# Optimization experiments

Measured on AMD Instinct MI355X. Metric: run time of the kernel, lower is better.

## Reference

```python
import jax, jax.numpy as jnp
import numpy as np

RES = 128
SH_DIM = 9            # (deg+1)^2, deg=2
CH = SH_DIM * 3 + 1   # 28: 3*9 SH rgb coeffs + 1 sigma
AABB_MIN = -1.0
AABB_MAX = 1.0
STEP = (AABB_MAX - AABB_MIN) / (RES - 1)   # voxel_len = mean(aabb_size/(res-1))
UNIFORM = 0.5
N_SAMPLES = int(RES * 3 / UNIFORM)         # plenoxels count: 768
EPS = 1e-10


def sh_encode_deg2(d):
    # real spherical harmonics basis, degree 2 (9 coefficients), on normalized dirs
    d = d / jnp.linalg.norm(d, axis=-1, keepdims=True)
    x, y, z = d[..., 0], d[..., 1], d[..., 2]
    C0 = 0.28209479177387814
    C1 = 0.4886025119029199
    C20, C21, C22 = 1.0925484305920792, -1.0925484305920792, 0.31539156525252005
    C23, C24 = -1.0925484305920792, 0.5462742152960396
    return jnp.stack([
        jnp.full_like(x, C0),
        -C1 * y, C1 * z, -C1 * x,
        C20 * x * y, C21 * y * z, C22 * (2.0 * z * z - x * x - y * y),
        C23 * x * z, C24 * (x * x - y * y),
    ], axis=-1)


def grid_sample_3d(grid, pts):
    # grid: [D,H,W,C]; pts: [...,3] in [-1,1], (x,y,z) with x->W, y->H, z->D.
    # Matches torch F.grid_sample(mode='bilinear', padding_mode='zeros', align_corners=True).
    D, H, W, C = grid.shape
    lead = pts.shape[:-1]
    p = pts.reshape(-1, 3)
    x = (p[:, 0] + 1.0) * 0.5 * (W - 1)
    y = (p[:, 1] + 1.0) * 0.5 * (H - 1)
    z = (p[:, 2] + 1.0) * 0.5 * (D - 1)
    x0f, y0f, z0f = jnp.floor(x), jnp.floor(y), jnp.floor(z)
    fx, fy, fz = x - x0f, y - y0f, z - z0f
    x0 = x0f.astype(jnp.int32)
    y0 = y0f.astype(jnp.int32)
    z0 = z0f.astype(jnp.int32)
    flat = grid.reshape(-1, C)
    out = jnp.zeros((p.shape[0], C), grid.dtype)
    for dz in (0, 1):
        for dy in (0, 1):
            for dx in (0, 1):
                xi, yi, zi = x0 + dx, y0 + dy, z0 + dz
                valid = (xi >= 0) & (xi < W) & (yi >= 0) & (yi < H) & (zi >= 0) & (zi < D)
                w = ((fx if dx else 1.0 - fx)
                     * (fy if dy else 1.0 - fy)
                     * (fz if dz else 1.0 - fz)) * valid
                idx = (jnp.clip(zi, 0, D - 1) * H + jnp.clip(yi, 0, H - 1)) * W + jnp.clip(xi, 0, W - 1)
                out = out + w[:, None] * flat[idx]
    return out.reshape(lead + (C,))


def setup_inputs() -> dict:
    key = jax.random.key(0)
    k1, k2, k3 = jax.random.split(key, 3)
    B = 4096
    # origins on a radius-3 sphere, aimed at jittered targets inside the unit box
    o = jax.random.normal(k1, (B, 3), dtype=jnp.float32)
    rays_o = 3.0 * o / jnp.linalg.norm(o, axis=-1, keepdims=True)
    tgt = jax.random.uniform(k2, (B, 3), dtype=jnp.float32, minval=-0.5, maxval=0.5)
    d = tgt - rays_o
    rays_d = d / jnp.linalg.norm(d, axis=-1, keepdims=True)
    grid_data = 0.1 * jax.random.normal(k3, (RES ** 3, CH), dtype=jnp.float32)
    grid_data = grid_data.at[:, -1].add(0.1)  # ini_sigma offset
    return {"rays_d": rays_d, "rays_o": rays_o, "grid_data": grid_data}


def reference(rays_d, rays_o, grid_data):
    B = rays_d.shape[0]
    aabb_lo = jnp.full((3,), AABB_MIN, rays_o.dtype)
    aabb_hi = jnp.full((3,), AABB_MAX, rays_o.dtype)
    # ray-AABB intersection (no_grad in torch)
    t_pos = (aabb_hi - rays_o) / rays_d
    t_neg = (aabb_lo - rays_o) / rays_d
    t_in = jnp.minimum(t_pos, t_neg)
    t_out = jnp.maximum(t_pos, t_neg)
    start = jnp.max(t_in, axis=-1)                  # [B]
    stop = jnp.min(t_out, axis=-1, keepdims=True)   # [B,1]
    # tensor_linspace from start+u*step to start+u*step*n, then clamp max=stop
    w = jnp.linspace(0.0, 1.0, N_SAMPLES, dtype=rays_o.dtype)  # [S]
    s0 = start + UNIFORM * STEP
    s1 = start + UNIFORM * STEP * N_SAMPLES
    intersections = s0[:, None] * (1.0 - w) + s1[:, None] * w   # [B,S]
    intersections = jnp.minimum(intersections, stop)
    t = intersections[:, :-1]                                    # [B,S-1]
    pts = rays_o[:, None, :] + t[:, :, None] * rays_d[:, None, :]
    pts = (pts - AABB_MIN) * (2.0 / (AABB_MAX - AABB_MIN)) - 1.0  # normalize to [-1,1]
    # trilinear sample of the voxel grid (torch layout: D=res0,H=res1,W=res2; x->W)
    interp = grid_sample_3d(grid_data.reshape(RES, RES, RES, CH), pts)  # [B,S-1,CH]
    sigma = interp[..., -1]
    rgb_sh = interp[..., :-1].reshape(B, N_SAMPLES - 1, 3, SH_DIM)
    sh = sh_encode_deg2(rays_d)                                   # [B,9]
    rgb = jnp.einsum('bsck,bk->bsc', rgb_sh, sh)
    # volumetric rendering
    dists = jnp.diff(intersections, axis=1) * jnp.linalg.norm(rays_d, axis=-1, keepdims=True)
    alpha = 1.0 - jnp.exp(-jax.nn.relu(sigma) * dists)
    cum_light = jnp.concatenate(
        [jnp.ones((B, 1), alpha.dtype), jnp.cumprod(1.0 - alpha[:, :-1] + EPS, axis=-1)], axis=-1)
    abs_light = alpha * cum_light
    acc_map = abs_light.sum(-1)
    rgb_map = (abs_light[..., None] * jax.nn.sigmoid(rgb)).sum(-2)
    depth = (abs_light * t).sum(-1)
    rgb_map = rgb_map + (1.0 - acc_map[:, None])  # white background
    return rgb_map, alpha, depth
```

## Files before the change

kernel.cpp:

```cpp
#include <hip/hip_runtime.h>
#include <math.h>

#define RESG 128
#define CHG 28
#define NT 767

__global__ __launch_bounds__(256) void nerf_grid_kernel(
    const float* __restrict__ rays_d,
    const float* __restrict__ rays_o,
    const float* __restrict__ grid,
    float* __restrict__ out_rgb,
    float* __restrict__ out_alpha,
    float* __restrict__ out_depth)
{
    const int ray  = blockIdx.x;
    const int tid  = threadIdx.x;
    const int lane = tid & 63;
    const int wave = tid >> 6;

    const float EPSC   = 1e-10f;
    const float INV127 = 1.0f / 127.0f;

    __shared__ float a_lds[NT + 1];
    __shared__ float r_lds[NT + 1];
    __shared__ float g_lds[NT + 1];
    __shared__ float b_lds[NT + 1];
    __shared__ float wprod[4];
    __shared__ float red[4][5];

    const float ox = rays_o[ray*3+0], oy = rays_o[ray*3+1], oz = rays_o[ray*3+2];
    const float dx = rays_d[ray*3+0], dy = rays_d[ray*3+1], dz = rays_d[ray*3+2];
    const float dnorm = sqrtf(dx*dx + dy*dy + dz*dz);

    float txp = (1.0f - ox)/dx, txn = (-1.0f - ox)/dx;
    float typ = (1.0f - oy)/dy, tyn = (-1.0f - oy)/dy;
    float tzp = (1.0f - oz)/dz, tzn = (-1.0f - oz)/dz;
    const float start = fmaxf(fmaxf(fminf(txp,txn), fminf(typ,tyn)), fminf(tzp,tzn));
    const float stop  = fminf(fminf(fmaxf(txp,txn), fmaxf(typ,tyn)), fmaxf(tzp,tzn));

    int n_proc = (int)((stop - start) * 127.0f) + 2;
    n_proc = n_proc < 0 ? 0 : (n_proc > NT ? NT : n_proc);

    const float inv = 1.0f/dnorm;
    const float nx = dx*inv, ny = dy*inv, nz = dz*inv;
    float sh0, sh1, sh2, sh3, sh4, sh5, sh6, sh7, sh8;
    {
        const float C0 = 0.28209479177387814f;
        const float C1 = 0.4886025119029199f;
        const float C20 = 1.0925484305920792f, C21 = -1.0925484305920792f;
        const float C22 = 0.31539156525252005f;
        const float C23 = -1.0925484305920792f, C24 = 0.5462742152960396f;
        sh0 = C0;
        sh1 = -C1*ny;
        sh2 =  C1*nz;
        sh3 = -C1*nx;
        sh4 = C20*nx*ny;
        sh5 = C21*ny*nz;
        sh6 = C22*(2.0f*nz*nz - nx*nx - ny*ny);
        sh7 = C23*nx*nz;
        sh8 = C24*(nx*nx - ny*ny);
    }

    const int samp   = lane >> 3;
    const int corner = lane & 7;
    const int cdx = corner & 1, cdy = (corner >> 1) & 1, cdz = corner >> 2;

    for (int base = wave*8; base < n_proc; base += 32) {
        const int s = base + samp;
        float rr = 0.0f, gg = 0.0f, bb = 0.0f, sg = 0.0f;
        float t0 = 0.0f, dist = 0.0f;
        bool live = false;
        if (s < n_proc) {
            t0 = fminf(start + (float)(s+1)*INV127, stop);
            const float t1 = fminf(start + (float)(s+2)*INV127, stop);
            dist = (t1 - t0) * dnorm;
            live = dist > 0.0f;
        }
        if (live) {
            const float gx = (ox + t0*dx + 1.0f)*63.5f;
            const float gy = (oy + t0*dy + 1.0f)*63.5f;
            const float gz = (oz + t0*dz + 1.0f)*63.5f;
            const float fx0 = floorf(gx), fy0 = floorf(gy), fz0 = floorf(gz);
            const float fx = gx - fx0, fy = gy - fy0, fz = gz - fz0;
            const int xi = (int)fx0 + cdx;
            const int yi = (int)fy0 + cdy;
            const int zi = (int)fz0 + cdz;
            const bool valid = ((unsigned)xi < (unsigned)RESG) &
                               ((unsigned)yi < (unsigned)RESG) &
                               ((unsigned)zi < (unsigned)RESG);
            const float w = (cdx ? fx : 1.0f-fx) *
                            (cdy ? fy : 1.0f-fy) *
                            (cdz ? fz : 1.0f-fz);
            if (valid && w != 0.0f) {
                const float4* row = (const float4*)(grid + (size_t)(((zi*RESG) + yi)*RESG + xi)*CHG);
                const float4 v0 = row[0], v1 = row[1], v2 = row[2], v3 = row[3];
                const float4 v4 = row[4], v5 = row[5], v6 = row[6];
                rr = w*(v0.x*sh0 + v0.y*sh1 + v0.z*sh2 + v0.w*sh3 +
                        v1.x*sh4 + v1.y*sh5 + v1.z*sh6 + v1.w*sh7 + v2.x*sh8);
                gg = w*(v2.y*sh0 + v2.z*sh1 + v2.w*sh2 + v3.x*sh3 +
                        v3.y*sh4 + v3.z*sh5 + v3.w*sh6 + v4.x*sh7 + v4.y*sh8);
                bb = w*(v4.z*sh0 + v4.w*sh1 + v5.x*sh2 + v5.y*sh3 +
                        v5.z*sh4 + v5.w*sh5 + v6.x*sh6 + v6.y*sh7 + v6.z*sh8);
                sg = w*v6.w;
            }
        }
        #pragma unroll
        for (int off = 1; off < 8; off <<= 1) {
            rr += __shfl_xor(rr, off, 64);
            gg += __shfl_xor(gg, off, 64);
            bb += __shfl_xor(bb, off, 64);
            sg += __shfl_xor(sg, off, 64);
        }
        if (corner == 0 && s < n_proc) {
            const float a = live ? 1.0f - expf(-fmaxf(sg, 0.0f)*dist) : 0.0f;
            a_lds[s] = a;
            r_lds[s] = 1.0f/(1.0f + expf(-rr));
            g_lds[s] = 1.0f/(1.0f + expf(-gg));
            b_lds[s] = 1.0f/(1.0f + expf(-bb));
        }
    }
    __syncthreads();

    for (int s = tid; s < NT; s += 256)
        out_alpha[(size_t)ray*NT + s] = (s < n_proc) ? a_lds[s] : 0.0f;

    float a_r[3], q_r[3], t_r[3], rr_r[3], gg_r[3], bb_r[3];
    #pragma unroll
    for (int k = 0; k < 3; ++k) {
        const int s = tid*3 + k;
        float a = 0.0f, rr = 0.0f, gg = 0.0f, bb = 0.0f, tt = 0.0f;
        if (s < NT) {
            tt = fminf(start + (float)(s+1)*INV127, stop);
            if (s < n_proc) {
                a  = a_lds[s];
                rr = r_lds[s]; gg = g_lds[s]; bb = b_lds[s];
            }
        }
        a_r[k] = a; q_r[k] = (s < NT) ? (1.0f - a + EPSC) : 1.0f;
        t_r[k] = tt; rr_r[k] = rr; gg_r[k] = gg; bb_r[k] = bb;
    }

    const float P = q_r[0]*q_r[1]*q_r[2];
    float incl = P;
    #pragma unroll
    for (int off = 1; off < 64; off <<= 1) {
        const float n = __shfl_up(incl, off, 64);
        if (lane >= off) incl *= n;
    }
    float excl = __shfl_up(incl, 1, 64);
    if (lane == 0) excl = 1.0f;

    if (lane == 63) wprod[wave] = incl;
    __syncthreads();
    float wpre = 1.0f;
    for (int w2 = 0; w2 < 4; ++w2) if (w2 < wave) wpre *= wprod[w2];

    float cum = wpre * excl;
    float accA = 0.0f, accR = 0.0f, accG = 0.0f, accB = 0.0f, accD = 0.0f;
    #pragma unroll
    for (int k = 0; k < 3; ++k) {
        const float abs_l = a_r[k] * cum;
        accA += abs_l;
        accR += abs_l * rr_r[k];
        accG += abs_l * gg_r[k];
        accB += abs_l * bb_r[k];
        accD += abs_l * t_r[k];
        cum *= q_r[k];
    }

    #pragma unroll
    for (int off = 32; off > 0; off >>= 1) {
        accA += __shfl_down(accA, off, 64);
        accR += __shfl_down(accR, off, 64);
        accG += __shfl_down(accG, off, 64);
        accB += __shfl_down(accB, off, 64);
        accD += __shfl_down(accD, off, 64);
    }
    if (lane == 0) {
        red[wave][0] = accA; red[wave][1] = accR; red[wave][2] = accG;
        red[wave][3] = accB; red[wave][4] = accD;
    }
    __syncthreads();
    if (tid == 0) {
        float A = 0.0f, R = 0.0f, G = 0.0f, Bv = 0.0f, D = 0.0f;
        #pragma unroll
        for (int w2 = 0; w2 < 4; ++w2) {
            A += red[w2][0]; R += red[w2][1]; G += red[w2][2];
            Bv += red[w2][3]; D += red[w2][4];
        }
        const float bg = 1.0f - A;
        out_rgb[ray*3+0] = R  + bg;
        out_rgb[ray*3+1] = G  + bg;
        out_rgb[ray*3+2] = Bv + bg;
        out_depth[ray] = D;
    }
}

extern "C" void kernel_launch(void* const* d_in, const int* in_sizes, int n_in,
                              void* d_out, int out_size, void* d_ws, size_t ws_size,
                              hipStream_t stream) {
    const float* rays_d = (const float*)d_in[0];
    const float* rays_o = (const float*)d_in[1];
    const float* grid   = (const float*)d_in[2];
    const int B = in_sizes[0] / 3;

    float* out       = (float*)d_out;
    float* out_rgb   = out;
    float* out_alpha = out + (size_t)B*3;
    float* out_depth = out + (size_t)B*3 + (size_t)B*NT;

    nerf_grid_kernel<<<B, 256, 0, stream>>>(rays_d, rays_o, grid,
                                            out_rgb, out_alpha, out_depth);
}
```

Before: 85.96 us.

## Sort rays by direction bucket, coalesce voxel gathers via LDS staging, bf16 colors

Adds a single-block prep kernel that buckets rays by cube-face direction and launches the main kernel in that permuted order, aiming for better L2 locality across concurrently running blocks. The voxel gather is restructured so each wave loads the 8×28-float rows cooperatively with lane-contiguous float4 loads into a rotated LDS staging buffer, then reads them back per corner. Sigmoid colors are stored in LDS as bf16, and the three exp/sigmoid evaluations are split across lanes. This adds block-wide barriers per iteration, an extra launch, a serial single-block sort, and a loss of color precision.

Measured after the change: 132.2 us. +53.7%, slower.

```diff
diff --git a/kernel.cpp b/kernel.cpp
--- a/kernel.cpp
+++ b/kernel.cpp
@@ -4,16 +4,63 @@
 #define RESG 128
 #define CHG 28
 #define NT 767
-
-__global__ __launch_bounds__(256) void nerf_grid_kernel(
+#define NBKT 96
+
+static __device__ __forceinline__ unsigned short f2bf(float x) {
+    unsigned u = __float_as_uint(x);
+    return (unsigned short)((u + 0x7FFFu + ((u >> 16) & 1u)) >> 16);
+}
+static __device__ __forceinline__ float bf2f(unsigned short h) {
+    return __uint_as_float(((unsigned)h) << 16);
+}
+
+__global__ __launch_bounds__(1024) void prep_sort(
+    const float* __restrict__ rays_d, int* __restrict__ perm, int B)
+{
+    __shared__ int cnt[NBKT];
+    __shared__ int off[NBKT];
+    __shared__ unsigned char keys[4096];
+    const int tid = threadIdx.x;
+    for (int i = tid; i < NBKT; i += 1024) cnt[i] = 0;
+    __syncthreads();
+    for (int r = tid; r < B; r += 1024) {
+        float ddx = rays_d[r*3+0], ddy = rays_d[r*3+1], ddz = rays_d[r*3+2];
+        float ax = fabsf(ddx), ay = fabsf(ddy), az = fabsf(ddz);
+        int face; float u, v, m;
+        if (ax >= ay && ax >= az) { face = (ddx < 0.f) ? 0 : 1; m = ax; u = ddy; v = ddz; }
+        else if (ay >= az)        { face = (ddy < 0.f) ? 2 : 3; m = ay; u = ddx; v = ddz; }
+        else                      { face = (ddz < 0.f) ? 4 : 5; m = az; u = ddx; v = ddy; }
+        float iu = u / m * 0.5f + 0.5f;
+        float iv = v / m * 0.5f + 0.5f;
+        int qu = min(3, max(0, (int)(iu * 4.0f)));
+        int qv = min(3, max(0, (int)(iv * 4.0f)));
+        int k = face * 16 + qu * 4 + qv;
+        keys[r] = (unsigned char)k;
+        atomicAdd(&cnt[k], 1);
+    }
+    __syncthreads();
+    if (tid == 0) {
+        int a = 0;
+        for (int i = 0; i < NBKT; ++i) { off[i] = a; a += cnt[i]; }
+    }
+    __syncthreads();
+    for (int r = tid; r < B; r += 1024) {
+        int k = keys[r];
+        int slot = atomicAdd(&off[k], 1);
+        perm[slot] = r;
+    }
+}
+
+__global__ __launch_bounds__(256, 4) void nerf_grid_kernel(
     const float* __restrict__ rays_d,
     const float* __restrict__ rays_o,
     const float* __restrict__ grid,
+    const int*   __restrict__ perm,
     float* __restrict__ out_rgb,
     float* __restrict__ out_alpha,
     float* __restrict__ out_depth)
 {
-    const int ray  = blockIdx.x;
+    const int ray  = perm[blockIdx.x];
     const int tid  = threadIdx.x;
     const int lane = tid & 63;
     const int wave = tid >> 6;
@@ -21,10 +68,10 @@
     const float EPSC   = 1e-10f;
     const float INV127 = 1.0f / 127.0f;
 
+    __shared__ float stage[4][1792];
     __shared__ float a_lds[NT + 1];
-    __shared__ float r_lds[NT + 1];
-    __shared__ float g_lds[NT + 1];
-    __shared__ float b_lds[NT + 1];
+    __shared__ unsigned int   rg_lds[NT + 1];
+    __shared__ unsigned short b_lds[NT + 1];
     __shared__ float wprod[4];
     __shared__ float red[4][5];
 
@@ -50,74 +97,94 @@
         const float C20 = 1.0925484305920792f, C21 = -1.0925484305920792f;
         const float C22 = 0.31539156525252005f;
         const float C23 = -1.0925484305920792f, C24 = 0.5462742152960396f;
-        sh0 = C0;
-        sh1 = -C1*ny;
-        sh2 =  C1*nz;
-        sh3 = -C1*nx;
-        sh4 = C20*nx*ny;
-        sh5 = C21*ny*nz;
+        sh0 = C0;   sh1 = -C1*ny; sh2 = C1*nz; sh3 = -C1*nx;
+        sh4 = C20*nx*ny; sh5 = C21*ny*nz;
         sh6 = C22*(2.0f*nz*nz - nx*nx - ny*ny);
-        sh7 = C23*nx*nz;
-        sh8 = C24*(nx*nx - ny*ny);
+        sh7 = C23*nx*nz; sh8 = C24*(nx*nx - ny*ny);
     }
 
     const int samp   = lane >> 3;
     const int corner = lane & 7;
     const int cdx = corner & 1, cdy = (corner >> 1) & 1, cdz = corner >> 2;
-
-    for (int base = wave*8; base < n_proc; base += 32) {
-        const int s = base + samp;
-        float rr = 0.0f, gg = 0.0f, bb = 0.0f, sg = 0.0f;
-        float t0 = 0.0f, dist = 0.0f;
-        bool live = false;
+    const char* gridc = (const char*)grid;
+
+    for (int base = 0; base < n_proc; base += 32) {
+        const int s = base + wave*8 + samp;
+        const float t0 = fminf(start + (float)(s+1)*INV127, stop);
+        const float t1 = fminf(start + (float)(s+2)*INV127, stop);
+        const float dist = (t1 - t0) * dnorm;
+        const bool on = (s < n_proc) && (dist > 0.0f);
+
+        const float gx = (ox + t0*dx + 1.0f)*63.5f;
+        const float gy = (oy + t0*dy + 1.0f)*63.5f;
+        const float gz = (oz + t0*dz + 1.0f)*63.5f;
+        const float fx0 = floorf(gx), fy0 = floorf(gy), fz0 = floorf(gz);
+        const float fx = gx - fx0, fy = gy - fy0, fz = gz - fz0;
+        const int ix = (int)fx0 + cdx;
+        const int iy = (int)fy0 + cdy;
+        const int iz = (int)fz0 + cdz;
+        const bool valid = on & ((unsigned)ix < (unsigned)RESG)
+                              & ((unsigned)iy < (unsigned)RESG)
+                              & ((unsigned)iz < (unsigned)RESG);
+        const int xc = min(RESG-1, max(0, ix));
+        const int yc = min(RESG-1, max(0, iy));
+        const int zc = min(RESG-1, max(0, iz));
+        const unsigned gb = (unsigned)(((zc*RESG + yc)*RESG + xc) * 112);
+        const float w = valid ? (cdx ? fx : 1.0f-fx) *
+                                (cdy ? fy : 1.0f-fy) *
+                                (cdz ? fz : 1.0f-fz) : 0.0f;
+
+        #pragma unroll
+        for (int i = 0; i < 7; ++i) {
+            const int g = i*64 + lane;
+            const int slot = (g * 18725) >> 17;
+            const int ch   = g - slot*7;
+            const unsigned gbv = (unsigned)__shfl((int)gb, slot, 64);
+            const float4 v = *(const float4*)(gridc + (size_t)gbv + (size_t)(ch << 4));
+            const int rs  = ch + slot;
+            const int rot = rs - 7*((rs * 18725) >> 17);
+            *(float4*)(&stage[wave][slot*28 + rot*4]) = v;
+        }
+        __syncthreads();
+
+        float4 c0, c1, c2, c3, c4, c5, c6;
+        {
+            int rs, rot;
+            rs = 0 + lane; rot = rs - 7*((rs*18725)>>17); c0 = *(const float4*)(&stage[wave][lane*28 + rot*4]);
+            rs = 1 + lane; rot = rs - 7*((rs*18725)>>17); c1 = *(const float4*)(&stage[wave][lane*28 + rot*4]);
+            rs = 2 + lane; rot = rs - 7*((rs*18725)>>17); c2 = *(const float4*)(&stage[wave][lane*28 + rot*4]);
+            rs = 3 + lane; rot = rs - 7*((rs*18725)>>17); c3 = *(const float4*)(&stage[wave][lane*28 + rot*4]);
+            rs = 4 + lane; rot = rs - 7*((rs*18725)>>17); c4 = *(const float4*)(&stage[wave][lane*28 + rot*4]);
+            rs = 5 + lane; rot = rs - 7*((rs*18725)>>17); c5 = *(const float4*)(&stage[wave][lane*28 + rot*4]);
+            rs = 6 + lane; rot = rs - 7*((rs*18725)>>17); c6 = *(const float4*)(&stage[wave][lane*28 + rot*4]);
+        }
+        float rr = w*(c0.x*sh0 + c0.y*sh1 + c0.z*sh2 + c0.w*sh3 +
+                      c1.x*sh4 + c1.y*sh5 + c1.z*sh6 + c1.w*sh7 + c2.x*sh8);
+        float gg = w*(c2.y*sh0 + c2.z*sh1 + c2.w*sh2 + c3.x*sh3 +
+                      c3.y*sh4 + c3.z*sh5 + c3.w*sh6 + c4.x*sh7 + c4.y*sh8);
+        float bb = w*(c4.z*sh0 + c4.w*sh1 + c5.x*sh2 + c5.y*sh3 +
+                      c5.z*sh4 + c5.w*sh5 + c6.x*sh6 + c6.y*sh7 + c6.z*sh8);
+        float sg = w*c6.w;
+
+        #pragma unroll
+        for (int off2 = 1; off2 < 8; off2 <<= 1) {
+            rr += __shfl_xor(rr, off2, 64);
+            gg += __shfl_xor(gg, off2, 64);
+            bb += __shfl_xor(bb, off2, 64);
+            sg += __shfl_xor(sg, off2, 64);
+        }
         if (s < n_proc) {
-            t0 = fminf(start + (float)(s+1)*INV127, stop);
-            const float t1 = fminf(start + (float)(s+2)*INV127, stop);
-            dist = (t1 - t0) * dnorm;
-            live = dist > 0.0f;
-        }
-        if (live) {
-            const float gx = (ox + t0*dx + 1.0f)*63.5f;
-            const float gy = (oy + t0*dy + 1.0f)*63.5f;
-            const float gz = (oz + t0*dz + 1.0f)*63.5f;
-            const float fx0 = floorf(gx), fy0 = floorf(gy), fz0 = floorf(gz);
-            const float fx = gx - fx0, fy = gy - fy0, fz = gz - fz0;
-            const int xi = (int)fx0 + cdx;
-            const int yi = (int)fy0 + cdy;
-            const int zi = (int)fz0 + cdz;
-            const bool valid = ((unsigned)xi < (unsigned)RESG) &
-                               ((unsigned)yi < (unsigned)RESG) &
-                               ((unsigned)zi < (unsigned)RESG);
-            const float w = (cdx ? fx : 1.0f-fx) *
-                            (cdy ? fy : 1.0f-fy) *
-                            (cdz ? fz : 1.0f-fz);
-            if (valid && w != 0.0f) {
-                const float4* row = (const float4*)(grid + (size_t)(((zi*RESG) + yi)*RESG + xi)*CHG);
-                const float4 v0 = row[0], v1 = row[1], v2 = row[2], v3 = row[3];
-                const float4 v4 = row[4], v5 = row[5], v6 = row[6];
-                rr = w*(v0.x*sh0 + v0.y*sh1 + v0.z*sh2 + v0.w*sh3 +
-                        v1.x*sh4 + v1.y*sh5 + v1.z*sh6 + v1.w*sh7 + v2.x*sh8);
-                gg = w*(v2.y*sh0 + v2.z*sh1 + v2.w*sh2 + v3.x*sh3 +
-                        v3.y*sh4 + v3.z*sh5 + v3.w*sh6 + v4.x*sh7 + v4.y*sh8);
-                bb = w*(v4.z*sh0 + v4.w*sh1 + v5.x*sh2 + v5.y*sh3 +
-                        v5.z*sh4 + v5.w*sh5 + v6.x*sh6 + v6.y*sh7 + v6.z*sh8);
-                sg = w*v6.w;
+            if (corner == 0) {
+                a_lds[s] = 1.0f - expf(-fmaxf(sg, 0.0f)*dist);
+            } else if (corner == 1) {
+                const float r1 = 1.0f/(1.0f + expf(-rr));
+                const float g1 = 1.0f/(1.0f + expf(-gg));
+                rg_lds[s] = ((unsigned)f2bf(r1) << 16) | (unsigned)f2bf(g1);
+            } else if (corner == 2) {
+                b_lds[s] = f2bf(1.0f/(1.0f + expf(-bb)));
             }
         }
-        #pragma unroll
-        for (int off = 1; off < 8; off <<= 1) {
-            rr += __shfl_xor(rr, off, 64);
-            gg += __shfl_xor(gg, off, 64);
-            bb += __shfl_xor(bb, off, 64);
-            sg += __shfl_xor(sg, off, 64);
-        }
-        if (corner == 0 && s < n_proc) {
-            const float a = live ? 1.0f - expf(-fmaxf(sg, 0.0f)*dist) : 0.0f;
-            a_lds[s] = a;
-            r_lds[s] = 1.0f/(1.0f + expf(-rr));
-            g_lds[s] = 1.0f/(1.0f + expf(-gg));
-            b_lds[s] = 1.0f/(1.0f + expf(-bb));
-        }
+        __syncthreads();
     }
     __syncthreads();
 
@@ -132,8 +199,11 @@
         if (s < NT) {
             tt = fminf(start + (float)(s+1)*INV127, stop);
             if (s < n_proc) {
-                a  = a_lds[s];
-                rr = r_lds[s]; gg = g_lds[s]; bb = b_lds[s];
+                a = a_lds[s];
+                const unsigned rg = rg_lds[s];
+                rr = bf2f((unsigned short)(rg >> 16));
+                gg = bf2f((unsigned short)(rg & 0xFFFFu));
+                bb = bf2f(b_lds[s]);
             }
         }
         a_r[k] = a; q_r[k] = (s < NT) ? (1.0f - a + EPSC) : 1.0f;
@@ -143,9 +213,9 @@
     const float P = q_r[0]*q_r[1]*q_r[2];
     float incl = P;
     #pragma unroll
-    for (int off = 1; off < 64; off <<= 1) {
-        const float n = __shfl_up(incl, off, 64);
-        if (lane >= off) incl *= n;
+    for (int off2 = 1; off2 < 64; off2 <<= 1) {
+        const float n = __shfl_up(incl, off2, 64);
+        if (lane >= off2) incl *= n;
     }
     float excl = __shfl_up(incl, 1, 64);
     if (lane == 0) excl = 1.0f;
@@ -169,12 +239,12 @@
     }
 
     #pragma unroll
-    for (int off = 32; off > 0; off >>= 1) {
-        accA += __shfl_down(accA, off, 64);
-        accR += __shfl_down(accR, off, 64);
-        accG += __shfl_down(accG, off, 64);
-        accB += __shfl_down(accB, off, 64);
-        accD += __shfl_down(accD, off, 64);
+    for (int off2 = 32; off2 > 0; off2 >>= 1) {
+        accA += __shfl_down(accA, off2, 64);
+        accR += __shfl_down(accR, off2, 64);
+        accG += __shfl_down(accG, off2, 64);
+        accB += __shfl_down(accB, off2, 64);
+        accD += __shfl_down(accD, off2, 64);
     }
     if (lane == 0) {
         red[wave][0] = accA; red[wave][1] = accR; red[wave][2] = accG;
@@ -209,6 +279,9 @@
     float* out_alpha = out + (size_t)B*3;
     float* out_depth = out + (size_t)B*3 + (size_t)B*NT;
 
-    nerf_grid_kernel<<<B, 256, 0, stream>>>(rays_d, rays_o, grid,
+    int* perm = (int*)d_ws;
+
+    prep_sort<<<1, 1024, 0, stream>>>(rays_d, perm, B);
+    nerf_grid_kernel<<<B, 256, 0, stream>>>(rays_d, rays_o, grid, perm,
                                             out_rgb, out_alpha, out_depth);
 }
```
